# Kernel optimization log

Hardware: AMD Instinct MI355X
Metric: run time of the kernel (lower is better)

The kernel has to match this reference:

```python
import jax, jax.numpy as jnp
import numpy as np

B, R, C, NH = 8, 64, 256, 8
N = R * R            # 4096 tokens
HD = C // NH         # head dim 32
FF = 3               # focusing factor

def dwconv(x, w, b):
    # x: (B, C, H, W); w: (C, 1, kh, kw) depthwise
    y = jax.lax.conv_general_dilated(
        x, w, window_strides=(1, 1), padding='SAME',
        dimension_numbers=('NCHW', 'OIHW', 'NCHW'),
        feature_group_count=x.shape[1])
    return y + b[None, :, None, None]

def setup_inputs() -> dict:
    key = jax.random.key(0)
    ks = jax.random.split(key, 6)
    return {
        'qkv': jax.random.normal(ks[0], (3, B, N, C), jnp.float32),
        'pos_enc': jax.random.normal(ks[1], (1, N, C), jnp.float32) * 0.02,
        'scale': jax.random.normal(ks[2], (1, 1, C), jnp.float32) * 0.02,
        'w_v': jax.random.normal(ks[3], (C, 1, 3, 3), jnp.float32) * 0.1,
        'b_v': jnp.zeros((C,), jnp.float32),
        'w_dwc': jax.random.normal(ks[4], (HD, 1, 5, 5), jnp.float32) * 0.1,
        'b_dwc': jnp.zeros((HD,), jnp.float32),
    }

def reference(qkv, pos_enc, scale, w_v, b_v, w_dwc, b_dwc):
    q, k, v = qkv[0], qkv[1], qkv[2]          # each (B, N, C)
    # --- LePE: depthwise 3x3 conv on v over full channel dim ---
    v_img = v.transpose(0, 2, 1).reshape(B, C, R, R)
    lepe = dwconv(v_img, w_v, b_v)            # (B, C, R, R)
    lepe = lepe.reshape(B * NH, HD, N).transpose(0, 2, 1)   # (B*h, N, hd)
    v = v_img.reshape(B, C, N).transpose(0, 2, 1)           # (B, N, C)
    # --- focused kernelization ---
    k = k + pos_enc
    sc = jax.nn.softplus(scale)
    q = (jax.nn.relu(q) + 1e-6) / sc
    k = (jax.nn.relu(k) + 1e-6) / sc
    qn = jnp.linalg.norm(q, axis=-1, keepdims=True)
    kn = jnp.linalg.norm(k, axis=-1, keepdims=True)
    q = q ** FF
    k = k ** FF
    q = q / jnp.linalg.norm(q, axis=-1, keepdims=True) * qn
    k = k / jnp.linalg.norm(k, axis=-1, keepdims=True) * kn
    split = lambda x: x.reshape(B, N, NH, HD).transpose(0, 2, 1, 3).reshape(B * NH, N, HD)
    q, k, v = split(q), split(k), split(v)    # (B*h, N, hd)
    # --- linear attention (kv aggregation path: N >> hd) ---
    z = 1.0 / (jnp.einsum('bic,bc->bi', q, k.sum(axis=1)) + 1e-6)
    kv = jnp.einsum('bjc,bjd->bcd', k, v)     # (B*h, hd, hd)
    x = jnp.einsum('bic,bcd,bi->bid', q, kv, z)
    # --- dwc feature mixing on v per head ---
    fm = v.transpose(0, 2, 1).reshape(B * NH, HD, R, R)
    fm = dwconv(fm, w_dwc, b_dwc).reshape(B * NH, HD, N).transpose(0, 2, 1)
    x = x + fm + lepe
    x = x.reshape(B, NH, N, HD).transpose(0, 2, 1, 3).reshape(B, N, C)
    return x
```

## Files before the change

### kernel.cpp

```cpp
#include <hip/hip_runtime.h>
#include <math.h>

#define B_  8
#define R_  64
#define C_  256
#define NH_ 8
#define N_  4096
#define HD_ 32

__device__ __forceinline__ float softplus_rcp(float s) {
    return 1.f / __logf(1.f + __expf(s));
}

__device__ __forceinline__ void gload16_lds(const float* g, float* l) {
    __builtin_amdgcn_global_load_lds(
        (const __attribute__((address_space(1))) unsigned int*)g,
        (__attribute__((address_space(3))) unsigned int*)l, 16, 0, 0);
}

__global__ __launch_bounds__(256, 2) void kernelNB7(
        const float* __restrict__ qkv, const float* __restrict__ pos,
        const float* __restrict__ scale,
        float* __restrict__ qs_arr, float* __restrict__ part,
        float* __restrict__ kspart) {
    __shared__ float smem[8448];
    float* rsc_s = smem + 8192;

    const int t    = threadIdx.x;
    const int wave = t >> 6, lane = t & 63;
    const int tk   = lane >> 5;
    const int lr   = lane & 31;
    const int blk  = blockIdx.x;
    const int tok0 = blk * 32;
    const int row  = wave * 2 + tk;

    rsc_s[t] = softplus_rcp(scale[t]);

    const size_t qbase = (size_t)tok0 * C_;
    const size_t koff  = (size_t)B_ * N_ * C_;
    const size_t voff  = (size_t)2 * B_ * N_ * C_;

    const int h  = t >> 5;
    const int l  = t & 31;
    const int cg = l & 7;
    const int dg = l >> 3;

    float acc[4][8];
    #pragma unroll
    for (int ii = 0; ii < 4; ii++)
        #pragma unroll
        for (int jj = 0; jj < 8; jj++) acc[ii][jj] = 0.f;
    float ksp[4] = {0.f, 0.f, 0.f, 0.f};

    float4 sq[2], sk[2], sp[2];
    float  rs[8];

    auto LOAD = [&](int tt) {
        float* vdst = smem + 4096 + (tt & 1) * 2048;
        const int r0 = wave * 2;
        const size_t vsrc = voff + qbase + (size_t)(tt * 8 + r0) * C_;
        gload16_lds(qkv + vsrc + lane * 4,      vdst + r0 * 256 + lane * 4);
        gload16_lds(qkv + vsrc + C_ + lane * 4, vdst + (r0 + 1) * 256 + lane * 4);
        const int    nrow = tt * 8 + row;
        const size_t off  = qbase + (size_t)nrow * C_;
        const size_t poff = (size_t)((tok0 + nrow) & (N_ - 1)) * C_;
        sq[0] = *(const float4*)(qkv + off + lr * 4);
        sq[1] = *(const float4*)(qkv + off + 128 + lr * 4);
        sk[0] = *(const float4*)(qkv + koff + off + lr * 4);
        sk[1] = *(const float4*)(qkv + koff + off + 128 + lr * 4);
        sp[0] = *(const float4*)(pos + poff + lr * 4);
        sp[1] = *(const float4*)(pos + poff + 128 + lr * 4);
    };

    auto PROC = [&](int tt) {
        float* kf_s = smem + (tt & 1) * 2048;
        const int tok = tok0 + tt * 8 + row;
        float kc[8];
        float sq2 = 0.f, sq6 = 0.f, sk2 = 0.f, sk6 = 0.f;
        #pragma unroll
        for (int j = 0; j < 2; j++) {
            const float qa[4] = {sq[j].x, sq[j].y, sq[j].z, sq[j].w};
            const float ka[4] = {sk[j].x, sk[j].y, sk[j].z, sk[j].w};
            const float pa[4] = {sp[j].x, sp[j].y, sp[j].z, sp[j].w};
            #pragma unroll
            for (int e = 0; e < 4; e++) {
                const float r  = rs[j * 4 + e];
                const float qv = (fmaxf(qa[e], 0.f) + 1e-6f) * r;
                const float kw = (fmaxf(ka[e] + pa[e], 0.f) + 1e-6f) * r;
                sq2 += qv * qv;  sk2 += kw * kw;
                const float q3 = qv * qv * qv, k3 = kw * kw * kw;
                sq6 += q3 * q3;  sk6 += k3 * k3;
                kc[j * 4 + e] = k3;
            }
        }
        #pragma unroll
        for (int m = 1; m < 32; m <<= 1) {
            sq2 += __shfl_xor(sq2, m, 64);
            sq6 += __shfl_xor(sq6, m, 64);
            sk2 += __shfl_xor(sk2, m, 64);
            sk6 += __shfl_xor(sk6, m, 64);
        }
        if (lr == 0) qs_arr[tok] = sqrtf(sq2) * rsqrtf(sq6);
        const float ks = sqrtf(sk2) * rsqrtf(sk6);
        #pragma unroll
        for (int j = 0; j < 2; j++) {
            const float4 kf4 = make_float4(kc[j*4+0] * ks, kc[j*4+1] * ks,
                                           kc[j*4+2] * ks, kc[j*4+3] * ks);
            *(float4*)&kf_s[row * 256 + j * 128 + lr * 4] = kf4;
        }
    };

    auto COMP = [&](int tt) {
        const float* kf_s = smem + (tt & 1) * 2048;
        const float* v_s  = smem + 4096 + (tt & 1) * 2048;
        const float* kfp = kf_s + h * HD_ + cg * 4;
        const float* vp  = v_s  + h * HD_ + dg * 8;
        #pragma unroll
        for (int nl = 0; nl < 8; nl++) {
            const float4 kr = *(const float4*)(kfp + nl * 256);
            const float4 va = *(const float4*)(vp  + nl * 256);
            const float4 vb = *(const float4*)(vp  + nl * 256 + 4);
            ksp[0] += kr.x;  ksp[1] += kr.y;
            ksp[2] += kr.z;  ksp[3] += kr.w;
            const float kk[4] = {kr.x, kr.y, kr.z, kr.w};
            const float vv[8] = {va.x, va.y, va.z, va.w,
                                 vb.x, vb.y, vb.z, vb.w};
            #pragma unroll
            for (int ii = 0; ii < 4; ii++)
                #pragma unroll
                for (int jj = 0; jj < 8; jj++)
                    acc[ii][jj] = fmaf(kk[ii], vv[jj], acc[ii][jj]);
        }
    };

    LOAD(0);
    __syncthreads();
    #pragma unroll
    for (int j = 0; j < 2; j++)
        *(float4*)&rs[j * 4] = *(const float4*)&rsc_s[j * 128 + lr * 4];
    PROC(0);
    LOAD(1);
    __syncthreads();
    #pragma unroll
    for (int tt = 0; tt < 4; tt++) {
        COMP(tt);
        if (tt < 3) PROC(tt + 1);
        __syncthreads();
        if (tt < 2) LOAD(tt + 2);
    }

    #pragma unroll
    for (int ii = 0; ii < 4; ii++) {
        const float4 a = make_float4(acc[ii][0], acc[ii][1], acc[ii][2], acc[ii][3]);
        const float4 b = make_float4(acc[ii][4], acc[ii][5], acc[ii][6], acc[ii][7]);
        const int base = h * 1024 + (cg * 4 + ii) * 32 + dg * 8;
        *(float4*)&smem[base]     = a;
        *(float4*)&smem[base + 4] = b;
    }
    if (dg == 0)
        *(float4*)&kspart[(size_t)blk * 256 + h * 32 + cg * 4] =
            make_float4(ksp[0], ksp[1], ksp[2], ksp[3]);
    __syncthreads();
    float* pdst = part + (size_t)blk * 8192;
    #pragma unroll
    for (int i = 0; i < 8; i++)
        *(float4*)&pdst[i * 1024 + t * 4] = *(const float4*)&smem[i * 1024 + t * 4];
}

__global__ __launch_bounds__(256) void kernelR(
        const float* __restrict__ part, const float* __restrict__ kspart,
        float* __restrict__ kv_ws, float* __restrict__ ksum_ws) {
    const int t  = threadIdx.x;
    const int bh = blockIdx.x >> 2, q = blockIdx.x & 3;
    const int b  = bh >> 3, h = bh & 7;

    const float* p = part + (size_t)(b * 128) * 8192 + h * 1024 + q * 256 + t;
    float s = 0.f;
    #pragma unroll 4
    for (int j = 0; j < 128; j++) s += p[(size_t)j * 8192];
    kv_ws[bh * 1024 + q * 256 + t] = s;

    if (q == 0 && t < 32) {
        const float* kp = kspart + (size_t)(b * 128) * 256 + h * 32 + t;
        float s2 = 0.f;
        #pragma unroll 8
        for (int j = 0; j < 128; j++) s2 += kp[(size_t)j * 256];
        ksum_ws[bh * 32 + t] = s2;
    }
}

__global__ __launch_bounds__(256) void kernelCD3(
        const float* __restrict__ qkv, const float* __restrict__ qs_arr,
        const float* __restrict__ kv_ws, const float* __restrict__ ksum_ws,
        const float* __restrict__ scale,
        const float* __restrict__ w_v,  const float* __restrict__ b_v,
        const float* __restrict__ w_dwc, const float* __restrict__ b_dwc,
        float* __restrict__ out) {
    __shared__ float v_s[20 * 20 * 32];
    __shared__ float rsc_s[32];
    const int t    = threadIdx.x;
    const int tile = blockIdx.x;
    const int h    = blockIdx.y;
    const int b    = blockIdx.z;
    const int ty0  = (tile >> 2) * 16, tx0 = (tile & 3) * 16;
    const int bh   = b * NH_ + h;

    const float4 kvr = ((const float4*)(kv_ws + (size_t)bh * 1024))[t];
    float ksr = 0.f;
    if (t < 32) {
        ksr      = ksum_ws[bh * HD_ + t];
        rsc_s[t] = softplus_rcp(scale[h * HD_ + t]);
    }

    const float* vb = qkv + (size_t)2 * B_ * N_ * C_ + (size_t)b * N_ * C_ + h * HD_;
    #pragma unroll
    for (int i = 0; i < 13; i++) {
        const int idx = i * 256 + t;
        if (idx < 3200) {
            const int pix = idx >> 3, d4 = (idx & 7) * 4;
            const int yy = pix / 20, xx = pix - yy * 20;
            const int gy = ty0 + yy - 2, gx = tx0 + xx - 2;
            float4 val = make_float4(0.f, 0.f, 0.f, 0.f);
            if (gy >= 0 && gy < R_ && gx >= 0 && gx < R_)
                val = *(const float4*)(vb + (size_t)(gy * R_ + gx) * C_ + d4);
            *(float4*)&v_s[pix * 32 + d4] = val;
        }
    }

    const int c  = t & 31, pg = t >> 5;
    float wv[9], wd[25];
    {
        const float* wvp = w_v + (size_t)(h * HD_ + c) * 9;
        const float* wdp = w_dwc + (size_t)c * 25;
        #pragma unroll
        for (int i = 0; i < 9; i++)  wv[i] = wvp[i];
        #pragma unroll
        for (int i = 0; i < 25; i++) wd[i] = wdp[i];
    }
    const float bias = b_v[h * HD_ + c] + b_dwc[c];
    __syncthreads();

    float res[32];
    #pragma unroll
    for (int r2 = 0; r2 < 2; r2++) {
        const int ty = pg * 2 + r2;
        float win[5][5];
        #pragma unroll
        for (int j = 0; j < 5; j++)
            #pragma unroll
            for (int i = 0; i < 5; i++)
                win[j][i] = v_s[((ty + i) * 20 + j) * 32 + c];
        #pragma unroll
        for (int tx = 0; tx < 16; tx++) {
            float a = bias;
            #pragma unroll
            for (int j = 0; j < 5; j++) {
                const int slot = (tx + j) % 5;
                #pragma unroll
                for (int i = 0; i < 5; i++)
                    a = fmaf(wd[i * 5 + j], win[slot][i], a);
            }
            #pragma unroll
            for (int j = 1; j < 4; j++) {
                const int slot = (tx + j) % 5;
                #pragma unroll
                for (int i = 1; i < 4; i++)
                    a = fmaf(wv[(i - 1) * 3 + (j - 1)], win[slot][i], a);
            }
            res[r2 * 16 + tx] = a;
            if (tx < 15) {
                const int slot = tx % 5;
                #pragma unroll
                for (int i = 0; i < 5; i++)
                    win[slot][i] = v_s[((ty + i) * 20 + (tx + 5)) * 32 + c];
            }
        }
    }
    __syncthreads();
    #pragma unroll
    for (int r2 = 0; r2 < 2; r2++)
        #pragma unroll
        for (int tx = 0; tx < 16; tx++)
            v_s[((pg * 2 + r2) * 16 + tx) * 33 + c] = res[r2 * 16 + tx];
    *(float4*)&v_s[8448 + t * 4] = kvr;
    if (t < 32) v_s[9472 + t] = ksr;
    __syncthreads();

    {
        const int tyy = t >> 4, txx = t & 15;
        const int n   = (ty0 + tyy) * R_ + (tx0 + txx);
        const int tok = b * N_ + n;
        float q[32];
        const float4* qsrc = (const float4*)(qkv + (size_t)tok * C_ + h * HD_);
        #pragma unroll
        for (int i = 0; i < 8; i++) ((float4*)q)[i] = qsrc[i];
        const float qs = qs_arr[tok];
        #pragma unroll
        for (int i = 0; i < 32; i++) {
            const float r = (fmaxf(q[i], 0.f) + 1e-6f) * rsc_s[i];
            q[i] = r * r * r * qs;
        }

        float denom = 1e-6f;
        #pragma unroll
        for (int cc = 0; cc < 32; cc++) denom = fmaf(q[cc], v_s[9472 + cc], denom);
        const float z = 1.f / denom;

        float o[32];
        #pragma unroll
        for (int i = 0; i < 32; i++) o[i] = 0.f;
        #pragma unroll
        for (int cc = 0; cc < 32; cc++) {
            const float qc = q[cc];
            #pragma unroll
            for (int d = 0; d < 32; d++)
                o[d] = fmaf(qc, v_s[8448 + cc * 32 + d], o[d]);
        }
        float4* dst = (float4*)(out + (size_t)tok * C_ + h * HD_);
        #pragma unroll
        for (int i = 0; i < 8; i++) {
            float4 v4;
            v4.x = fmaf(o[i*4+0], z, v_s[t * 33 + i*4+0]);
            v4.y = fmaf(o[i*4+1], z, v_s[t * 33 + i*4+1]);
            v4.z = fmaf(o[i*4+2], z, v_s[t * 33 + i*4+2]);
            v4.w = fmaf(o[i*4+3], z, v_s[t * 33 + i*4+3]);
            dst[i] = v4;
        }
    }
}

extern "C" void kernel_launch(void* const* d_in, const int* in_sizes, int n_in,
                              void* d_out, int out_size, void* d_ws, size_t ws_size,
                              hipStream_t stream) {
    const float* qkv   = (const float*)d_in[0];
    const float* pos   = (const float*)d_in[1];
    const float* scale = (const float*)d_in[2];
    const float* w_v   = (const float*)d_in[3];
    const float* b_v   = (const float*)d_in[4];
    const float* w_dwc = (const float*)d_in[5];
    const float* b_dwc = (const float*)d_in[6];
    float* out = (float*)d_out;

    float* qs_arr  = (float*)d_ws;
    float* part    = qs_arr + (size_t)B_ * N_;
    float* kspart  = part + (size_t)1024 * 8192;
    float* kv_ws   = kspart + (size_t)1024 * 256;
    float* ksum_ws = kv_ws + 64 * 1024;

    kernelNB7<<<dim3(1024), 256, 0, stream>>>(qkv, pos, scale, qs_arr, part, kspart);
    kernelR<<<dim3(256), 256, 0, stream>>>(part, kspart, kv_ws, ksum_ws);
    kernelCD3<<<dim3(16, NH_, B_), 256, 0, stream>>>(qkv, qs_arr, kv_ws, ksum_ws,
                                                     scale, w_v, b_v, w_dwc, b_dwc, out);
}
```

Before: 226.3 us.

## Move q-norm computation from KV kernel into reduction kernel; prefetch q early

```diff
diff --git a/kernel.cpp b/kernel.cpp
--- a/kernel.cpp
+++ b/kernel.cpp
@@ -18,11 +18,10 @@
         (__attribute__((address_space(3))) unsigned int*)l, 16, 0, 0);
 }
 
-__global__ __launch_bounds__(256, 2) void kernelNB7(
+__global__ __launch_bounds__(256) void kernelKV8(
         const float* __restrict__ qkv, const float* __restrict__ pos,
         const float* __restrict__ scale,
-        float* __restrict__ qs_arr, float* __restrict__ part,
-        float* __restrict__ kspart) {
+        float* __restrict__ part, float* __restrict__ kspart) {
     __shared__ float smem[8448];
     float* rsc_s = smem + 8192;
 
@@ -52,7 +51,7 @@
         for (int jj = 0; jj < 8; jj++) acc[ii][jj] = 0.f;
     float ksp[4] = {0.f, 0.f, 0.f, 0.f};
 
-    float4 sq[2], sk[2], sp[2];
+    float4 sk[2], sp[2];
     float  rs[8];
 
     auto LOAD = [&](int tt) {
@@ -64,8 +63,6 @@
         const int    nrow = tt * 8 + row;
         const size_t off  = qbase + (size_t)nrow * C_;
         const size_t poff = (size_t)((tok0 + nrow) & (N_ - 1)) * C_;
-        sq[0] = *(const float4*)(qkv + off + lr * 4);
-        sq[1] = *(const float4*)(qkv + off + 128 + lr * 4);
         sk[0] = *(const float4*)(qkv + koff + off + lr * 4);
         sk[1] = *(const float4*)(qkv + koff + off + 128 + lr * 4);
         sp[0] = *(const float4*)(pos + poff + lr * 4);
@@ -74,33 +71,27 @@
 
     auto PROC = [&](int tt) {
         float* kf_s = smem + (tt & 1) * 2048;
-        const int tok = tok0 + tt * 8 + row;
         float kc[8];
-        float sq2 = 0.f, sq6 = 0.f, sk2 = 0.f, sk6 = 0.f;
+        float sk2 = 0.f, sk6 = 0.f;
         #pragma unroll
         for (int j = 0; j < 2; j++) {
-            const float qa[4] = {sq[j].x, sq[j].y, sq[j].z, sq[j].w};
             const float ka[4] = {sk[j].x, sk[j].y, sk[j].z, sk[j].w};
             const float pa[4] = {sp[j].x, sp[j].y, sp[j].z, sp[j].w};
             #pragma unroll
             for (int e = 0; e < 4; e++) {
                 const float r  = rs[j * 4 + e];
-                const float qv = (fmaxf(qa[e], 0.f) + 1e-6f) * r;
                 const float kw = (fmaxf(ka[e] + pa[e], 0.f) + 1e-6f) * r;
-                sq2 += qv * qv;  sk2 += kw * kw;
-                const float q3 = qv * qv * qv, k3 = kw * kw * kw;
-                sq6 += q3 * q3;  sk6 += k3 * k3;
+                sk2 += kw * kw;
+                const float k3 = kw * kw * kw;
+                sk6 += k3 * k3;
                 kc[j * 4 + e] = k3;
             }
         }
         #pragma unroll
         for (int m = 1; m < 32; m <<= 1) {
-            sq2 += __shfl_xor(sq2, m, 64);
-            sq6 += __shfl_xor(sq6, m, 64);
             sk2 += __shfl_xor(sk2, m, 64);
             sk6 += __shfl_xor(sk6, m, 64);
         }
-        if (lr == 0) qs_arr[tok] = sqrtf(sq2) * rsqrtf(sq6);
         const float ks = sqrtf(sk2) * rsqrtf(sk6);
         #pragma unroll
         for (int j = 0; j < 2; j++) {
@@ -167,29 +158,74 @@
         *(float4*)&pdst[i * 1024 + t * 4] = *(const float4*)&smem[i * 1024 + t * 4];
 }
 
-__global__ __launch_bounds__(256) void kernelR(
+__global__ __launch_bounds__(256) void kernelRQ(
+        const float* __restrict__ qkv, const float* __restrict__ scale,
         const float* __restrict__ part, const float* __restrict__ kspart,
-        float* __restrict__ kv_ws, float* __restrict__ ksum_ws) {
-    const int t  = threadIdx.x;
-    const int bh = blockIdx.x >> 2, q = blockIdx.x & 3;
-    const int b  = bh >> 3, h = bh & 7;
-
-    const float* p = part + (size_t)(b * 128) * 8192 + h * 1024 + q * 256 + t;
-    float s = 0.f;
-    #pragma unroll 4
-    for (int j = 0; j < 128; j++) s += p[(size_t)j * 8192];
-    kv_ws[bh * 1024 + q * 256 + t] = s;
-
-    if (q == 0 && t < 32) {
-        const float* kp = kspart + (size_t)(b * 128) * 256 + h * 32 + t;
-        float s2 = 0.f;
-        #pragma unroll 8
-        for (int j = 0; j < 128; j++) s2 += kp[(size_t)j * 256];
-        ksum_ws[bh * 32 + t] = s2;
-    }
-}
-
-__global__ __launch_bounds__(256) void kernelCD3(
+        float* __restrict__ kv_ws, float* __restrict__ ksum_ws,
+        float* __restrict__ qs_arr) {
+    const int t   = threadIdx.x;
+    const int bid = blockIdx.x;
+
+    if (bid < 256) {
+        const int bh = bid >> 2, q = bid & 3;
+        const int b  = bh >> 3, h = bh & 7;
+        const float* p = part + (size_t)(b * 128) * 8192 + h * 1024 + q * 256 + t;
+        float s = 0.f;
+        #pragma unroll 4
+        for (int j = 0; j < 128; j++) s += p[(size_t)j * 8192];
+        kv_ws[bh * 1024 + q * 256 + t] = s;
+
+        if (q == 0 && t < 32) {
+            const float* kp = kspart + (size_t)(b * 128) * 256 + h * 32 + t;
+            float s2 = 0.f;
+            #pragma unroll 8
+            for (int j = 0; j < 128; j++) s2 += kp[(size_t)j * 256];
+            ksum_ws[bh * 32 + t] = s2;
+        }
+        return;
+    }
+
+    __shared__ float rsc_s[C_];
+    rsc_s[t] = softplus_rcp(scale[t]);
+    __syncthreads();
+
+    const int wave = t >> 6, lane = t & 63;
+    const int tk   = lane >> 4;
+    const int lr   = lane & 15;
+    const int tok0 = (bid - 256) * 64;
+
+    float rs[16];
+    #pragma unroll
+    for (int j = 0; j < 4; j++)
+        *(float4*)&rs[j * 4] = *(const float4*)&rsc_s[j * 64 + lr * 4];
+
+    #pragma unroll
+    for (int it = 0; it < 4; it++) {
+        const int tok = tok0 + it * 16 + wave * 4 + tk;
+        const float* src = qkv + (size_t)tok * C_;
+        float sq2 = 0.f, sq6 = 0.f;
+        #pragma unroll
+        for (int j = 0; j < 4; j++) {
+            const float4 q4 = *(const float4*)(src + j * 64 + lr * 4);
+            const float qa[4] = {q4.x, q4.y, q4.z, q4.w};
+            #pragma unroll
+            for (int e = 0; e < 4; e++) {
+                const float qv = (fmaxf(qa[e], 0.f) + 1e-6f) * rs[j * 4 + e];
+                sq2 += qv * qv;
+                const float q3 = qv * qv * qv;
+                sq6 += q3 * q3;
+            }
+        }
+        #pragma unroll
+        for (int m = 1; m < 16; m <<= 1) {
+            sq2 += __shfl_xor(sq2, m, 64);
+            sq6 += __shfl_xor(sq6, m, 64);
+        }
+        if (lr == 0) qs_arr[tok] = sqrtf(sq2) * rsqrtf(sq6);
+    }
+}
+
+__global__ __launch_bounds__(256) void kernelCD4(
         const float* __restrict__ qkv, const float* __restrict__ qs_arr,
         const float* __restrict__ kv_ws, const float* __restrict__ ksum_ws,
         const float* __restrict__ scale,
@@ -227,6 +263,17 @@
         }
     }
 
+    const int tyy = t >> 4, txx = t & 15;
+    const int n_  = (ty0 + tyy) * R_ + (tx0 + txx);
+    const int tok = b * N_ + n_;
+    float qreg[32];
+    {
+        const float4* qsrc = (const float4*)(qkv + (size_t)tok * C_ + h * HD_);
+        #pragma unroll
+        for (int i = 0; i < 8; i++) ((float4*)qreg)[i] = qsrc[i];
+    }
+    const float qs = qs_arr[tok];
+
     const int c  = t & 31, pg = t >> 5;
     float wv[9], wd[25];
     {
@@ -287,23 +334,15 @@
     __syncthreads();
 
     {
-        const int tyy = t >> 4, txx = t & 15;
-        const int n   = (ty0 + tyy) * R_ + (tx0 + txx);
-        const int tok = b * N_ + n;
-        float q[32];
-        const float4* qsrc = (const float4*)(qkv + (size_t)tok * C_ + h * HD_);
-        #pragma unroll
-        for (int i = 0; i < 8; i++) ((float4*)q)[i] = qsrc[i];
-        const float qs = qs_arr[tok];
         #pragma unroll
         for (int i = 0; i < 32; i++) {
-            const float r = (fmaxf(q[i], 0.f) + 1e-6f) * rsc_s[i];
-            q[i] = r * r * r * qs;
+            const float r = (fmaxf(qreg[i], 0.f) + 1e-6f) * rsc_s[i];
+            qreg[i] = r * r * r * qs;
         }
 
         float denom = 1e-6f;
         #pragma unroll
-        for (int cc = 0; cc < 32; cc++) denom = fmaf(q[cc], v_s[9472 + cc], denom);
+        for (int cc = 0; cc < 32; cc++) denom = fmaf(qreg[cc], v_s[9472 + cc], denom);
         const float z = 1.f / denom;
 
         float o[32];
@@ -311,7 +350,7 @@
         for (int i = 0; i < 32; i++) o[i] = 0.f;
         #pragma unroll
         for (int cc = 0; cc < 32; cc++) {
-            const float qc = q[cc];
+            const float qc = qreg[cc];
             #pragma unroll
             for (int d = 0; d < 32; d++)
                 o[d] = fmaf(qc, v_s[8448 + cc * 32 + d], o[d]);
@@ -347,8 +386,9 @@
     float* kv_ws   = kspart + (size_t)1024 * 256;
     float* ksum_ws = kv_ws + 64 * 1024;
 
-    kernelNB7<<<dim3(1024), 256, 0, stream>>>(qkv, pos, scale, qs_arr, part, kspart);
-    kernelR<<<dim3(256), 256, 0, stream>>>(part, kspart, kv_ws, ksum_ws);
-    kernelCD3<<<dim3(16, NH_, B_), 256, 0, stream>>>(qkv, qs_arr, kv_ws, ksum_ws,
+    kernelKV8<<<dim3(1024), 256, 0, stream>>>(qkv, pos, scale, part, kspart);
+    kernelRQ<<<dim3(768), 256, 0, stream>>>(qkv, scale, part, kspart,
+                                            kv_ws, ksum_ws, qs_arr);
+    kernelCD4<<<dim3(16, NH_, B_), 256, 0, stream>>>(qkv, qs_arr, kv_ws, ksum_ws,
                                                      scale, w_v, b_v, w_dwc, b_dwc, out);
 }
```

Measured after the change: 232.4 us. 1.03x slower.
